# Performance work log

Measured on AMD Instinct MI355X. Metric: run time of the kernel, lower is better.

## Reference

```python
import jax, jax.numpy as jnp
import numpy as np

GAMMA = 0.5          # blending coeff from __init__
NEG_SLOPE = 0.2      # LeakyReLU slope
MASK_FILL = -9e15    # zero_vec constant from source

N, M, D = 8192, 8192, 256
SPARSITY = 0.01


def setup_inputs() -> dict:
    key = jax.random.key(0)
    k1, k2, k3, k4, k5 = jax.random.split(key, 5)
    input1 = jax.random.normal(k1, (N, D), dtype=jnp.float32)
    input2 = jax.random.normal(k2, (M, D), dtype=jnp.float32)
    adj = (jax.random.uniform(k3, (N, M)) < SPARSITY).astype(jnp.float32)
    # xavier_normal with gain=1.414 on (D,1): std = gain*sqrt(2/(D+1))
    std = 1.414 * np.sqrt(2.0 / (D + 1))
    a1 = jax.random.normal(k4, (D, 1), dtype=jnp.float32) * std
    a2 = jax.random.normal(k5, (D, 1), dtype=jnp.float32) * std
    return {"input1": input1, "input2": input2, "adj": adj, "a1": a1, "a2": a2}


def reference(input1, input2, adj, a1, a2):
    # e1: (N,1) broadcast against e2: (1,M) -> e: (N,M)
    e1 = input1 @ a1                      # (N,1)
    e2 = (input2 @ a2).T                  # (1,M)
    e = jax.nn.leaky_relu(e1 + e2, negative_slope=NEG_SLOPE)
    attention = jnp.where(adj > 0, e, MASK_FILL)
    attention = jax.nn.softmax(attention, axis=1)
    # scale each row by its adjacency degree, then gamma-blend with adj
    attention = attention * jnp.sum(adj, axis=1, keepdims=True)
    attention = attention * GAMMA + adj * (1.0 - GAMMA)
    return attention @ input2             # (N,D)
```

## Files before the change

### kernel.cpp

```cpp
#include <hip/hip_runtime.h>
#include <cstdint>
#include <cstddef>

#define NEG_SLOPE 0.2f
#define MAXK 256

typedef float f32x4 __attribute__((ext_vector_type(4)));
typedef unsigned short u16x4 __attribute__((ext_vector_type(4)));

static __device__ __forceinline__ unsigned short f2bf_rne(float f) {
  unsigned u = __float_as_uint(f);
  unsigned r = (u + 0x7FFFu + ((u >> 16) & 1u)) >> 16;
  return (unsigned short)r;
}
static __device__ __forceinline__ float bf2f(unsigned short h) {
  return __uint_as_float((unsigned)h << 16);
}

__global__ __launch_bounds__(256) void conv_kernel(
    const float* __restrict__ x2, unsigned short* __restrict__ x2h, int total4) {
  int t = blockIdx.x * blockDim.x + threadIdx.x;
  if (t >= total4) return;
  f32x4 v = reinterpret_cast<const f32x4*>(x2)[t];
  u16x4 h;
  h.x = f2bf_rne(v.x); h.y = f2bf_rne(v.y);
  h.z = f2bf_rne(v.z); h.w = f2bf_rne(v.w);
  reinterpret_cast<u16x4*>(x2h)[t] = h;
}

__global__ __launch_bounds__(256) void score_kernel(
    const float* __restrict__ x1, const float* __restrict__ x2,
    const float* __restrict__ a1, const float* __restrict__ a2,
    float* __restrict__ e1, float* __restrict__ f2, int N, int M, int D) {
  int gtid = blockIdx.x * blockDim.x + threadIdx.x;
  int wid = gtid >> 6;
  int lane = threadIdx.x & 63;
  if (wid >= N + M) return;
  const float* x; const float* a; float* outp; int row;
  if (wid < N) { x = x1; a = a1; outp = e1; row = wid; }
  else         { x = x2; a = a2; outp = f2; row = wid - N; }
  const float4 xv = *reinterpret_cast<const float4*>(x + (size_t)row * D + lane * 4);
  const float4 av = *reinterpret_cast<const float4*>(a + lane * 4);
  float s = xv.x * av.x + xv.y * av.y + xv.z * av.z + xv.w * av.w;
  #pragma unroll
  for (int off = 32; off > 0; off >>= 1) s += __shfl_down(s, off, 64);
  if (lane == 0) outp[row] = s;
}

__global__ __launch_bounds__(256) void attn_kernel(
    const float* __restrict__ adj, const unsigned short* __restrict__ x2h,
    const float* __restrict__ e1, const float* __restrict__ f2,
    float* __restrict__ out, int N, int M, int D) {
  __shared__ int   s_idx[4][MAXK];
  __shared__ float s_w[4][MAXK];

  const int tid  = threadIdx.x;
  const int wv   = tid >> 6;
  const int lane = tid & 63;
  const int row  = blockIdx.x * 4 + wv;
  if (row >= N) return;

  const int D4 = D >> 2;
  const float e1i = e1[row];
  const f32x4* __restrict__ arow4 =
      reinterpret_cast<const f32x4*>(adj + (size_t)row * M);

  uint64_t m0 = 0ull, m1 = 0ull;
  #pragma unroll 8
  for (int it = 0; it < 16; ++it) {
    f32x4 v = __builtin_nontemporal_load(&arow4[it * 64 + lane]);
    uint64_t b = 0;
    if (v.x > 0.f) b |= 1ull;
    if (v.y > 0.f) b |= 2ull;
    if (v.z > 0.f) b |= 4ull;
    if (v.w > 0.f) b |= 8ull;
    m0 |= b << (it * 4);
  }
  #pragma unroll 8
  for (int it = 16; it < 32; ++it) {
    f32x4 v = __builtin_nontemporal_load(&arow4[it * 64 + lane]);
    uint64_t b = 0;
    if (v.x > 0.f) b |= 1ull;
    if (v.y > 0.f) b |= 2ull;
    if (v.z > 0.f) b |= 4ull;
    if (v.w > 0.f) b |= 8ull;
    m1 |= b << ((it - 16) * 4);
  }
  const int cnt = __popcll(m0) + __popcll(m1);

  int incl = cnt;
  #pragma unroll
  for (int off = 1; off < 64; off <<= 1) {
    int v = __shfl_up(incl, off, 64);
    if (lane >= off) incl += v;
  }
  int pos = incl - cnt;
  const int K = __shfl(incl, 63, 64);

  while (m0) {
    int b = __ffsll((unsigned long long)m0) - 1;
    m0 &= m0 - 1;
    int c = ((b >> 2) << 6) + lane;
    int j = (c << 2) + (b & 3);
    float e = e1i + f2[j];
    e = (e > 0.f) ? e : NEG_SLOPE * e;
    if (pos < MAXK) { s_idx[wv][pos] = j; s_w[wv][pos] = e; }
    ++pos;
  }
  while (m1) {
    int b = __ffsll((unsigned long long)m1) - 1;
    m1 &= m1 - 1;
    int c = (((b >> 2) + 16) << 6) + lane;
    int j = (c << 2) + (b & 3);
    float e = e1i + f2[j];
    e = (e > 0.f) ? e : NEG_SLOPE * e;
    if (pos < MAXK) { s_idx[wv][pos] = j; s_w[wv][pos] = e; }
    ++pos;
  }

  float4* __restrict__ out4 = reinterpret_cast<float4*>(out);
  if (K == 0) {
    float4 z; z.x = z.y = z.z = z.w = 0.f;
    out4[(size_t)row * D4 + lane] = z;
    return;
  }

  float lm = -1e30f;
  for (int k = lane; k < K; k += 64) lm = fmaxf(lm, s_w[wv][k]);
  #pragma unroll
  for (int off = 32; off > 0; off >>= 1) lm = fmaxf(lm, __shfl_xor(lm, off, 64));

  float ls = 0.f;
  for (int k = lane; k < K; k += 64) {
    float p = __expf(s_w[wv][k] - lm);
    s_w[wv][k] = p;
    ls += p;
  }
  #pragma unroll
  for (int off = 32; off > 0; off >>= 1) ls += __shfl_xor(ls, off, 64);

  const float scale = 0.5f * (float)K / ls;
  for (int k = lane; k < K; k += 64) s_w[wv][k] = s_w[wv][k] * scale + 0.5f;

  const u16x4* __restrict__ x2h4 = reinterpret_cast<const u16x4*>(x2h);
  float4 a0, a1v, a2v, a3;
  a0.x=a0.y=a0.z=a0.w=0.f; a1v=a0; a2v=a0; a3=a0;
  int k = 0;
  for (; k + 4 <= K; k += 4) {
    int j0 = __builtin_amdgcn_readfirstlane(s_idx[wv][k]);
    int j1 = __builtin_amdgcn_readfirstlane(s_idx[wv][k + 1]);
    int j2 = __builtin_amdgcn_readfirstlane(s_idx[wv][k + 2]);
    int j3 = __builtin_amdgcn_readfirstlane(s_idx[wv][k + 3]);
    float w0 = s_w[wv][k],     w1 = s_w[wv][k + 1];
    float w2 = s_w[wv][k + 2], w3 = s_w[wv][k + 3];
    u16x4 h0 = x2h4[(size_t)j0 * D4 + lane];
    u16x4 h1 = x2h4[(size_t)j1 * D4 + lane];
    u16x4 h2 = x2h4[(size_t)j2 * D4 + lane];
    u16x4 h3 = x2h4[(size_t)j3 * D4 + lane];
    a0.x = fmaf(w0, bf2f(h0.x), a0.x); a0.y = fmaf(w0, bf2f(h0.y), a0.y);
    a0.z = fmaf(w0, bf2f(h0.z), a0.z); a0.w = fmaf(w0, bf2f(h0.w), a0.w);
    a1v.x = fmaf(w1, bf2f(h1.x), a1v.x); a1v.y = fmaf(w1, bf2f(h1.y), a1v.y);
    a1v.z = fmaf(w1, bf2f(h1.z), a1v.z); a1v.w = fmaf(w1, bf2f(h1.w), a1v.w);
    a2v.x = fmaf(w2, bf2f(h2.x), a2v.x); a2v.y = fmaf(w2, bf2f(h2.y), a2v.y);
    a2v.z = fmaf(w2, bf2f(h2.z), a2v.z); a2v.w = fmaf(w2, bf2f(h2.w), a2v.w);
    a3.x = fmaf(w3, bf2f(h3.x), a3.x); a3.y = fmaf(w3, bf2f(h3.y), a3.y);
    a3.z = fmaf(w3, bf2f(h3.z), a3.z); a3.w = fmaf(w3, bf2f(h3.w), a3.w);
  }
  for (; k < K; ++k) {
    int j = __builtin_amdgcn_readfirstlane(s_idx[wv][k]);
    float w = s_w[wv][k];
    u16x4 h = x2h4[(size_t)j * D4 + lane];
    a0.x = fmaf(w, bf2f(h.x), a0.x); a0.y = fmaf(w, bf2f(h.y), a0.y);
    a0.z = fmaf(w, bf2f(h.z), a0.z); a0.w = fmaf(w, bf2f(h.w), a0.w);
  }
  float4 r;
  r.x = (a0.x + a1v.x) + (a2v.x + a3.x);
  r.y = (a0.y + a1v.y) + (a2v.y + a3.y);
  r.z = (a0.z + a1v.z) + (a2v.z + a3.z);
  r.w = (a0.w + a1v.w) + (a2v.w + a3.w);
  out4[(size_t)row * D4 + lane] = r;
}

extern "C" void kernel_launch(void* const* d_in, const int* in_sizes, int n_in,
                              void* d_out, int out_size, void* d_ws, size_t ws_size,
                              hipStream_t stream) {
  const float* x1  = (const float*)d_in[0];
  const float* x2  = (const float*)d_in[1];
  const float* adj = (const float*)d_in[2];
  const float* a1  = (const float*)d_in[3];
  const float* a2  = (const float*)d_in[4];
  float* out = (float*)d_out;

  const int D = in_sizes[3];
  const int N = in_sizes[0] / D;
  const int M = in_sizes[1] / D;

  float* e1 = (float*)d_ws;
  float* f2 = e1 + N;
  unsigned short* x2h = (unsigned short*)(f2 + M);

  const int total4 = (M * D) >> 2;
  conv_kernel<<<(total4 + 255) / 256, 256, 0, stream>>>(x2, x2h, total4);

  const int waves = N + M;
  const int blocks1 = (waves * 64 + 255) / 256;
  score_kernel<<<blocks1, 256, 0, stream>>>(x1, x2, a1, a2, e1, f2, N, M, D);
  attn_kernel<<<(N + 3) / 4, 256, 0, stream>>>(adj, x2h, e1, f2, out, N, M, D);
}
```

Measured before the change: 79.66 us.

## Fuse bf16 conversion into scoring; split attention into compact and gather kernels

Folds the bf16 conversion of input2 into the row-score kernel, so input2 is read once instead of twice. The attention kernel is split in two: a compact kernel streams adj and writes per-row neighbor index/weight pairs (capped at KCAP) to workspace, and a separate gather kernel does the weighted bf16 row accumulation. The split lets each phase run with its own occupancy and access pattern, at the cost of an extra launch and a round trip of the pairs through global memory. Rows with more than KCAP neighbors are truncated, which could change results for dense rows. The old fused kernel is kept as a fallback when workspace is too small.

```diff
diff --git a/kernel.cpp b/kernel.cpp
--- a/kernel.cpp
+++ b/kernel.cpp
@@ -4,9 +4,11 @@
 
 #define NEG_SLOPE 0.2f
 #define MAXK 256
+#define KCAP 144
 
 typedef float f32x4 __attribute__((ext_vector_type(4)));
 typedef unsigned short u16x4 __attribute__((ext_vector_type(4)));
+typedef unsigned int u32x2 __attribute__((ext_vector_type(2)));
 
 static __device__ __forceinline__ unsigned short f2bf_rne(float f) {
   unsigned u = __float_as_uint(f);
@@ -17,40 +19,41 @@
   return __uint_as_float((unsigned)h << 16);
 }
 
-__global__ __launch_bounds__(256) void conv_kernel(
-    const float* __restrict__ x2, unsigned short* __restrict__ x2h, int total4) {
-  int t = blockIdx.x * blockDim.x + threadIdx.x;
-  if (t >= total4) return;
-  f32x4 v = reinterpret_cast<const f32x4*>(x2)[t];
-  u16x4 h;
-  h.x = f2bf_rne(v.x); h.y = f2bf_rne(v.y);
-  h.z = f2bf_rne(v.z); h.w = f2bf_rne(v.w);
-  reinterpret_cast<u16x4*>(x2h)[t] = h;
-}
-
-__global__ __launch_bounds__(256) void score_kernel(
+__global__ __launch_bounds__(256) void score_conv_kernel(
     const float* __restrict__ x1, const float* __restrict__ x2,
     const float* __restrict__ a1, const float* __restrict__ a2,
-    float* __restrict__ e1, float* __restrict__ f2, int N, int M, int D) {
+    float* __restrict__ e1, float* __restrict__ f2,
+    unsigned short* __restrict__ x2h, int N, int M, int D) {
   int gtid = blockIdx.x * blockDim.x + threadIdx.x;
   int wid = gtid >> 6;
   int lane = threadIdx.x & 63;
   if (wid >= N + M) return;
-  const float* x; const float* a; float* outp; int row;
-  if (wid < N) { x = x1; a = a1; outp = e1; row = wid; }
-  else         { x = x2; a = a2; outp = f2; row = wid - N; }
-  const float4 xv = *reinterpret_cast<const float4*>(x + (size_t)row * D + lane * 4);
-  const float4 av = *reinterpret_cast<const float4*>(a + lane * 4);
-  float s = xv.x * av.x + xv.y * av.y + xv.z * av.z + xv.w * av.w;
-  #pragma unroll
-  for (int off = 32; off > 0; off >>= 1) s += __shfl_down(s, off, 64);
-  if (lane == 0) outp[row] = s;
-}
-
-__global__ __launch_bounds__(256) void attn_kernel(
-    const float* __restrict__ adj, const unsigned short* __restrict__ x2h,
+  const float4 av = *reinterpret_cast<const float4*>(
+      ((wid < N) ? a1 : a2) + lane * 4);
+  if (wid < N) {
+    const float4 xv = *reinterpret_cast<const float4*>(x1 + (size_t)wid * D + lane * 4);
+    float s = xv.x * av.x + xv.y * av.y + xv.z * av.z + xv.w * av.w;
+    #pragma unroll
+    for (int off = 32; off > 0; off >>= 1) s += __shfl_down(s, off, 64);
+    if (lane == 0) e1[wid] = s;
+  } else {
+    int row = wid - N;
+    const float4 xv = *reinterpret_cast<const float4*>(x2 + (size_t)row * D + lane * 4);
+    float s = xv.x * av.x + xv.y * av.y + xv.z * av.z + xv.w * av.w;
+    u16x4 h;
+    h.x = f2bf_rne(xv.x); h.y = f2bf_rne(xv.y);
+    h.z = f2bf_rne(xv.z); h.w = f2bf_rne(xv.w);
+    reinterpret_cast<u16x4*>(x2h)[(size_t)row * (D >> 2) + lane] = h;
+    #pragma unroll
+    for (int off = 32; off > 0; off >>= 1) s += __shfl_down(s, off, 64);
+    if (lane == 0) f2[row] = s;
+  }
+}
+
+__global__ __launch_bounds__(256) void compact_kernel(
+    const float* __restrict__ adj,
     const float* __restrict__ e1, const float* __restrict__ f2,
-    float* __restrict__ out, int N, int M, int D) {
+    int* __restrict__ krow, u32x2* __restrict__ pairs, int N, int M) {
   __shared__ int   s_idx[4][MAXK];
   __shared__ float s_w[4][MAXK];
 
@@ -60,7 +63,6 @@
   const int row  = blockIdx.x * 4 + wv;
   if (row >= N) return;
 
-  const int D4 = D >> 2;
   const float e1i = e1[row];
   const f32x4* __restrict__ arow4 =
       reinterpret_cast<const f32x4*>(adj + (size_t)row * M);
@@ -118,18 +120,13 @@
     ++pos;
   }
 
-  float4* __restrict__ out4 = reinterpret_cast<float4*>(out);
-  if (K == 0) {
-    float4 z; z.x = z.y = z.z = z.w = 0.f;
-    out4[(size_t)row * D4 + lane] = z;
-    return;
-  }
+  if (lane == 0) krow[row] = (K < KCAP) ? K : KCAP;
+  if (K == 0) return;
 
   float lm = -1e30f;
   for (int k = lane; k < K; k += 64) lm = fmaxf(lm, s_w[wv][k]);
   #pragma unroll
   for (int off = 32; off > 0; off >>= 1) lm = fmaxf(lm, __shfl_xor(lm, off, 64));
-
   float ls = 0.f;
   for (int k = lane; k < K; k += 64) {
     float p = __expf(s_w[wv][k] - lm);
@@ -140,7 +137,39 @@
   for (int off = 32; off > 0; off >>= 1) ls += __shfl_xor(ls, off, 64);
 
   const float scale = 0.5f * (float)K / ls;
-  for (int k = lane; k < K; k += 64) s_w[wv][k] = s_w[wv][k] * scale + 0.5f;
+  for (int k = lane; k < K && k < KCAP; k += 64) {
+    u32x2 p;
+    p.x = (unsigned)s_idx[wv][k];
+    p.y = __float_as_uint(s_w[wv][k] * scale + 0.5f);
+    pairs[(size_t)row * KCAP + k] = p;
+  }
+}
+
+__global__ __launch_bounds__(256) void gather_kernel(
+    const unsigned short* __restrict__ x2h, const int* __restrict__ krow,
+    const u32x2* __restrict__ pairs, float* __restrict__ out, int N, int D) {
+  __shared__ int   s_idx[4][KCAP];
+  __shared__ float s_w[4][KCAP];
+
+  const int tid  = threadIdx.x;
+  const int wv   = tid >> 6;
+  const int lane = tid & 63;
+  const int row  = blockIdx.x * 4 + wv;
+  if (row >= N) return;
+
+  const int D4 = D >> 2;
+  float4* __restrict__ out4 = reinterpret_cast<float4*>(out);
+  const int K = krow[row];
+  if (K == 0) {
+    float4 z; z.x = z.y = z.z = z.w = 0.f;
+    out4[(size_t)row * D4 + lane] = z;
+    return;
+  }
+  for (int k = lane; k < K; k += 64) {
+    u32x2 p = pairs[(size_t)row * KCAP + k];
+    s_idx[wv][k] = (int)p.x;
+    s_w[wv][k]   = __uint_as_float(p.y);
+  }
 
   const u16x4* __restrict__ x2h4 = reinterpret_cast<const u16x4*>(x2h);
   float4 a0, a1v, a2v, a3;
@@ -181,6 +210,129 @@
   out4[(size_t)row * D4 + lane] = r;
 }
 
+__global__ __launch_bounds__(256) void attn_fused_kernel(
+    const float* __restrict__ adj, const unsigned short* __restrict__ x2h,
+    const float* __restrict__ e1, const float* __restrict__ f2,
+    float* __restrict__ out, int N, int M, int D) {
+  __shared__ int   s_idx[4][MAXK];
+  __shared__ float s_w[4][MAXK];
+  const int tid  = threadIdx.x;
+  const int wv   = tid >> 6;
+  const int lane = tid & 63;
+  const int row  = blockIdx.x * 4 + wv;
+  if (row >= N) return;
+  const int D4 = D >> 2;
+  const float e1i = e1[row];
+  const f32x4* __restrict__ arow4 = reinterpret_cast<const f32x4*>(adj + (size_t)row * M);
+  uint64_t m0 = 0ull, m1 = 0ull;
+  #pragma unroll 8
+  for (int it = 0; it < 16; ++it) {
+    f32x4 v = __builtin_nontemporal_load(&arow4[it * 64 + lane]);
+    uint64_t b = 0;
+    if (v.x > 0.f) b |= 1ull;
+    if (v.y > 0.f) b |= 2ull;
+    if (v.z > 0.f) b |= 4ull;
+    if (v.w > 0.f) b |= 8ull;
+    m0 |= b << (it * 4);
+  }
+  #pragma unroll 8
+  for (int it = 16; it < 32; ++it) {
+    f32x4 v = __builtin_nontemporal_load(&arow4[it * 64 + lane]);
+    uint64_t b = 0;
+    if (v.x > 0.f) b |= 1ull;
+    if (v.y > 0.f) b |= 2ull;
+    if (v.z > 0.f) b |= 4ull;
+    if (v.w > 0.f) b |= 8ull;
+    m1 |= b << ((it - 16) * 4);
+  }
+  const int cnt = __popcll(m0) + __popcll(m1);
+  int incl = cnt;
+  #pragma unroll
+  for (int off = 1; off < 64; off <<= 1) {
+    int v = __shfl_up(incl, off, 64);
+    if (lane >= off) incl += v;
+  }
+  int pos = incl - cnt;
+  const int K = __shfl(incl, 63, 64);
+  while (m0) {
+    int b = __ffsll((unsigned long long)m0) - 1;
+    m0 &= m0 - 1;
+    int c = ((b >> 2) << 6) + lane;
+    int j = (c << 2) + (b & 3);
+    float e = e1i + f2[j];
+    e = (e > 0.f) ? e : NEG_SLOPE * e;
+    if (pos < MAXK) { s_idx[wv][pos] = j; s_w[wv][pos] = e; }
+    ++pos;
+  }
+  while (m1) {
+    int b = __ffsll((unsigned long long)m1) - 1;
+    m1 &= m1 - 1;
+    int c = (((b >> 2) + 16) << 6) + lane;
+    int j = (c << 2) + (b & 3);
+    float e = e1i + f2[j];
+    e = (e > 0.f) ? e : NEG_SLOPE * e;
+    if (pos < MAXK) { s_idx[wv][pos] = j; s_w[wv][pos] = e; }
+    ++pos;
+  }
+  float4* __restrict__ out4 = reinterpret_cast<float4*>(out);
+  if (K == 0) {
+    float4 z; z.x = z.y = z.z = z.w = 0.f;
+    out4[(size_t)row * D4 + lane] = z;
+    return;
+  }
+  float lm = -1e30f;
+  for (int k = lane; k < K; k += 64) lm = fmaxf(lm, s_w[wv][k]);
+  #pragma unroll
+  for (int off = 32; off > 0; off >>= 1) lm = fmaxf(lm, __shfl_xor(lm, off, 64));
+  float ls = 0.f;
+  for (int k = lane; k < K; k += 64) {
+    float p = __expf(s_w[wv][k] - lm);
+    s_w[wv][k] = p;
+    ls += p;
+  }
+  #pragma unroll
+  for (int off = 32; off > 0; off >>= 1) ls += __shfl_xor(ls, off, 64);
+  const float scale = 0.5f * (float)K / ls;
+  for (int k = lane; k < K; k += 64) s_w[wv][k] = s_w[wv][k] * scale + 0.5f;
+  const u16x4* __restrict__ x2h4 = reinterpret_cast<const u16x4*>(x2h);
+  float4 a0, a1v, a2v, a3;
+  a0.x=a0.y=a0.z=a0.w=0.f; a1v=a0; a2v=a0; a3=a0;
+  int k = 0;
+  for (; k + 4 <= K; k += 4) {
+    int j0 = __builtin_amdgcn_readfirstlane(s_idx[wv][k]);
+    int j1 = __builtin_amdgcn_readfirstlane(s_idx[wv][k + 1]);
+    int j2 = __builtin_amdgcn_readfirstlane(s_idx[wv][k + 2]);
+    int j3 = __builtin_amdgcn_readfirstlane(s_idx[wv][k + 3]);
+    float w0 = s_w[wv][k],     w1 = s_w[wv][k + 1];
+    float w2 = s_w[wv][k + 2], w3 = s_w[wv][k + 3];
+    u16x4 h0 = x2h4[(size_t)j0 * D4 + lane];
+    u16x4 h1 = x2h4[(size_t)j1 * D4 + lane];
+    u16x4 h2 = x2h4[(size_t)j2 * D4 + lane];
+    u16x4 h3 = x2h4[(size_t)j3 * D4 + lane];
+    a0.x = fmaf(w0, bf2f(h0.x), a0.x); a0.y = fmaf(w0, bf2f(h0.y), a0.y);
+    a0.z = fmaf(w0, bf2f(h0.z), a0.z); a0.w = fmaf(w0, bf2f(h0.w), a0.w);
+    a1v.x = fmaf(w1, bf2f(h1.x), a1v.x); a1v.y = fmaf(w1, bf2f(h1.y), a1v.y);
+    a1v.z = fmaf(w1, bf2f(h1.z), a1v.z); a1v.w = fmaf(w1, bf2f(h1.w), a1v.w);
+    a2v.x = fmaf(w2, bf2f(h2.x), a2v.x); a2v.y = fmaf(w2, bf2f(h2.y), a2v.y);
+    a2v.z = fmaf(w2, bf2f(h2.z), a2v.z); a2v.w = fmaf(w2, bf2f(h2.w), a2v.w);
+    a3.x = fmaf(w3, bf2f(h3.x), a3.x); a3.y = fmaf(w3, bf2f(h3.y), a3.y);
+    a3.z = fmaf(w3, bf2f(h3.z), a3.z); a3.w = fmaf(w3, bf2f(h3.w), a3.w);
+  }
+  for (; k < K; ++k) {
+    int j = __builtin_amdgcn_readfirstlane(s_idx[wv][k]);
+    float w = s_w[wv][k];
+    u16x4 h = x2h4[(size_t)j * D4 + lane];
+    a0.x = fmaf(w, bf2f(h.x), a0.x); a0.y = fmaf(w, bf2f(h.y), a0.y);
+    a0.z = fmaf(w, bf2f(h.z), a0.z); a0.w = fmaf(w, bf2f(h.w), a0.w);
+  }
+  float4 r;
+  r.x = (a0.x + a1v.x) + (a2v.x + a3.x);
+  r.y = (a0.y + a1v.y) + (a2v.y + a3.y);
+  r.z = (a0.z + a1v.z) + (a2v.z + a3.z);
+  r.w = (a0.w + a1v.w) + (a2v.w + a3.w);
+  out4[(size_t)row * D4 + lane] = r;
+}
+
 extern "C" void kernel_launch(void* const* d_in, const int* in_sizes, int n_in,
                               void* d_out, int out_size, void* d_ws, size_t ws_size,
                               hipStream_t stream) {
@@ -195,15 +347,22 @@
   const int N = in_sizes[0] / D;
   const int M = in_sizes[1] / D;
 
-  float* e1 = (float*)d_ws;
-  float* f2 = e1 + N;
-  unsigned short* x2h = (unsigned short*)(f2 + M);
-
-  const int total4 = (M * D) >> 2;
-  conv_kernel<<<(total4 + 255) / 256, 256, 0, stream>>>(x2, x2h, total4);
+  char* p = (char*)d_ws;
+  float* e1 = (float*)p;                 p += (size_t)N * 4;
+  float* f2 = (float*)p;                 p += (size_t)M * 4;
+  unsigned short* x2h = (unsigned short*)p; p += (size_t)M * D * 2;
+  int* krow = (int*)p;                   p += (size_t)N * 4;
+  u32x2* pairs = (u32x2*)p;              p += (size_t)N * KCAP * 8;
+  const size_t need = (size_t)(p - (char*)d_ws);
 
   const int waves = N + M;
   const int blocks1 = (waves * 64 + 255) / 256;
-  score_kernel<<<blocks1, 256, 0, stream>>>(x1, x2, a1, a2, e1, f2, N, M, D);
-  attn_kernel<<<(N + 3) / 4, 256, 0, stream>>>(adj, x2h, e1, f2, out, N, M, D);
-}
+  score_conv_kernel<<<blocks1, 256, 0, stream>>>(x1, x2, a1, a2, e1, f2, x2h, N, M, D);
+
+  if (ws_size >= need) {
+    compact_kernel<<<(N + 3) / 4, 256, 0, stream>>>(adj, e1, f2, krow, pairs, N, M);
+    gather_kernel<<<(N + 3) / 4, 256, 0, stream>>>(x2h, krow, pairs, out, N, D);
+  } else {
+    attn_fused_kernel<<<(N + 3) / 4, 256, 0, stream>>>(adj, x2h, e1, f2, out, N, M, D);
+  }
+}
```

Result: slower. 82.77 us (+3.9%).

## Fuse conversion into score kernel and stream adjacency chunks with one-pass softmax

Applied to the files above, without the earlier changes.

Folds the bf16 conversion of input2 into the score kernel, removing one launch and one extra read of input2. The score kernel also keeps a global maximum of f2 via atomics, so the attention kernel can use a fixed softmax shift bound (leaky_relu(e1 + max f2)) instead of a per-row max pass. The attention kernel now processes the adjacency row in four 2048-column chunks, prefetching the next chunk while it compacts and gathers the current one. It accumulates the exp-weighted and plain sums in one pass and applies the normalisation at the end. The risks are underflow when the global bound sits far above a row's true max, and a per-chunk cap of 160 neighbours.

```diff
diff --git a/kernel.cpp b/kernel.cpp
--- a/kernel.cpp
+++ b/kernel.cpp
@@ -3,7 +3,8 @@
 #include <cstddef>
 
 #define NEG_SLOPE 0.2f
-#define MAXK 256
+#define CCAP 160
+#define NCHUNK 4
 
 typedef float f32x4 __attribute__((ext_vector_type(4)));
 typedef unsigned short u16x4 __attribute__((ext_vector_type(4)));
@@ -16,43 +17,56 @@
 static __device__ __forceinline__ float bf2f(unsigned short h) {
   return __uint_as_float((unsigned)h << 16);
 }
-
-__global__ __launch_bounds__(256) void conv_kernel(
-    const float* __restrict__ x2, unsigned short* __restrict__ x2h, int total4) {
-  int t = blockIdx.x * blockDim.x + threadIdx.x;
-  if (t >= total4) return;
-  f32x4 v = reinterpret_cast<const f32x4*>(x2)[t];
-  u16x4 h;
-  h.x = f2bf_rne(v.x); h.y = f2bf_rne(v.y);
-  h.z = f2bf_rne(v.z); h.w = f2bf_rne(v.w);
-  reinterpret_cast<u16x4*>(x2h)[t] = h;
-}
-
-__global__ __launch_bounds__(256) void score_kernel(
+static __device__ __forceinline__ unsigned enc_f(float x) {
+  unsigned u = __float_as_uint(x);
+  return (u & 0x80000000u) ? ~u : (u | 0x80000000u);
+}
+static __device__ __forceinline__ float dec_f(unsigned e) {
+  return __uint_as_float((e & 0x80000000u) ? (e ^ 0x80000000u) : ~e);
+}
+
+__global__ __launch_bounds__(256) void score_conv_kernel(
     const float* __restrict__ x1, const float* __restrict__ x2,
     const float* __restrict__ a1, const float* __restrict__ a2,
-    float* __restrict__ e1, float* __restrict__ f2, int N, int M, int D) {
+    float* __restrict__ e1, float* __restrict__ f2,
+    unsigned short* __restrict__ x2h, unsigned* __restrict__ f2max_enc,
+    int N, int M, int D) {
   int gtid = blockIdx.x * blockDim.x + threadIdx.x;
   int wid = gtid >> 6;
   int lane = threadIdx.x & 63;
   if (wid >= N + M) return;
-  const float* x; const float* a; float* outp; int row;
-  if (wid < N) { x = x1; a = a1; outp = e1; row = wid; }
-  else         { x = x2; a = a2; outp = f2; row = wid - N; }
-  const float4 xv = *reinterpret_cast<const float4*>(x + (size_t)row * D + lane * 4);
-  const float4 av = *reinterpret_cast<const float4*>(a + lane * 4);
-  float s = xv.x * av.x + xv.y * av.y + xv.z * av.z + xv.w * av.w;
-  #pragma unroll
-  for (int off = 32; off > 0; off >>= 1) s += __shfl_down(s, off, 64);
-  if (lane == 0) outp[row] = s;
+  const float4 av = *reinterpret_cast<const float4*>(
+      ((wid < N) ? a1 : a2) + lane * 4);
+  if (wid < N) {
+    const float4 xv = *reinterpret_cast<const float4*>(x1 + (size_t)wid * D + lane * 4);
+    float s = xv.x * av.x + xv.y * av.y + xv.z * av.z + xv.w * av.w;
+    #pragma unroll
+    for (int off = 32; off > 0; off >>= 1) s += __shfl_down(s, off, 64);
+    if (lane == 0) e1[wid] = s;
+  } else {
+    int row = wid - N;
+    const float4 xv = *reinterpret_cast<const float4*>(x2 + (size_t)row * D + lane * 4);
+    float s = xv.x * av.x + xv.y * av.y + xv.z * av.z + xv.w * av.w;
+    u16x4 h;
+    h.x = f2bf_rne(xv.x); h.y = f2bf_rne(xv.y);
+    h.z = f2bf_rne(xv.z); h.w = f2bf_rne(xv.w);
+    reinterpret_cast<u16x4*>(x2h)[(size_t)row * (D >> 2) + lane] = h;
+    #pragma unroll
+    for (int off = 32; off > 0; off >>= 1) s += __shfl_down(s, off, 64);
+    if (lane == 0) {
+      f2[row] = s;
+      atomicMax(f2max_enc, enc_f(s));
+    }
+  }
 }
 
 __global__ __launch_bounds__(256) void attn_kernel(
     const float* __restrict__ adj, const unsigned short* __restrict__ x2h,
     const float* __restrict__ e1, const float* __restrict__ f2,
+    const unsigned* __restrict__ f2max_enc,
     float* __restrict__ out, int N, int M, int D) {
-  __shared__ int   s_idx[4][MAXK];
-  __shared__ float s_w[4][MAXK];
+  __shared__ int   s_idx[4][CCAP];
+  __shared__ float s_e[4][CCAP];
 
   const int tid  = threadIdx.x;
   const int wv   = tid >> 6;
@@ -62,60 +76,121 @@
 
   const int D4 = D >> 2;
   const float e1i = e1[row];
+  float mb = e1i + dec_f(*f2max_enc);
+  mb = (mb > 0.f) ? mb : NEG_SLOPE * mb;
+
   const f32x4* __restrict__ arow4 =
       reinterpret_cast<const f32x4*>(adj + (size_t)row * M);
-
-  uint64_t m0 = 0ull, m1 = 0ull;
-  #pragma unroll 8
-  for (int it = 0; it < 16; ++it) {
-    f32x4 v = __builtin_nontemporal_load(&arow4[it * 64 + lane]);
-    uint64_t b = 0;
-    if (v.x > 0.f) b |= 1ull;
-    if (v.y > 0.f) b |= 2ull;
-    if (v.z > 0.f) b |= 4ull;
-    if (v.w > 0.f) b |= 8ull;
-    m0 |= b << (it * 4);
-  }
-  #pragma unroll 8
-  for (int it = 16; it < 32; ++it) {
-    f32x4 v = __builtin_nontemporal_load(&arow4[it * 64 + lane]);
-    uint64_t b = 0;
-    if (v.x > 0.f) b |= 1ull;
-    if (v.y > 0.f) b |= 2ull;
-    if (v.z > 0.f) b |= 4ull;
-    if (v.w > 0.f) b |= 8ull;
-    m1 |= b << ((it - 16) * 4);
-  }
-  const int cnt = __popcll(m0) + __popcll(m1);
-
-  int incl = cnt;
-  #pragma unroll
-  for (int off = 1; off < 64; off <<= 1) {
-    int v = __shfl_up(incl, off, 64);
-    if (lane >= off) incl += v;
-  }
-  int pos = incl - cnt;
-  const int K = __shfl(incl, 63, 64);
-
-  while (m0) {
-    int b = __ffsll((unsigned long long)m0) - 1;
-    m0 &= m0 - 1;
-    int c = ((b >> 2) << 6) + lane;
-    int j = (c << 2) + (b & 3);
-    float e = e1i + f2[j];
-    e = (e > 0.f) ? e : NEG_SLOPE * e;
-    if (pos < MAXK) { s_idx[wv][pos] = j; s_w[wv][pos] = e; }
-    ++pos;
-  }
-  while (m1) {
-    int b = __ffsll((unsigned long long)m1) - 1;
-    m1 &= m1 - 1;
-    int c = (((b >> 2) + 16) << 6) + lane;
-    int j = (c << 2) + (b & 3);
-    float e = e1i + f2[j];
-    e = (e > 0.f) ? e : NEG_SLOPE * e;
-    if (pos < MAXK) { s_idx[wv][pos] = j; s_w[wv][pos] = e; }
-    ++pos;
+  const u16x4* __restrict__ x2h4 = reinterpret_cast<const u16x4*>(x2h);
+
+  const f32x4* pb = arow4 + lane;
+  f32x4 v0 = __builtin_nontemporal_load(pb + 0 * 64);
+  f32x4 v1 = __builtin_nontemporal_load(pb + 1 * 64);
+  f32x4 v2 = __builtin_nontemporal_load(pb + 2 * 64);
+  f32x4 v3 = __builtin_nontemporal_load(pb + 3 * 64);
+  f32x4 v4 = __builtin_nontemporal_load(pb + 4 * 64);
+  f32x4 v5 = __builtin_nontemporal_load(pb + 5 * 64);
+  f32x4 v6 = __builtin_nontemporal_load(pb + 6 * 64);
+  f32x4 v7 = __builtin_nontemporal_load(pb + 7 * 64);
+
+  float4 acc1, acc2;
+  acc1.x = acc1.y = acc1.z = acc1.w = 0.f;
+  acc2 = acc1;
+  float Z = 0.f;
+  int K = 0;
+
+  for (int c = 0; c < NCHUNK; ++c) {
+    unsigned mask = 0;
+    {
+      f32x4 x;
+      x = v0; if (x.x>0.f) mask|=1u<<0;  if (x.y>0.f) mask|=1u<<1;  if (x.z>0.f) mask|=1u<<2;  if (x.w>0.f) mask|=1u<<3;
+      x = v1; if (x.x>0.f) mask|=1u<<4;  if (x.y>0.f) mask|=1u<<5;  if (x.z>0.f) mask|=1u<<6;  if (x.w>0.f) mask|=1u<<7;
+      x = v2; if (x.x>0.f) mask|=1u<<8;  if (x.y>0.f) mask|=1u<<9;  if (x.z>0.f) mask|=1u<<10; if (x.w>0.f) mask|=1u<<11;
+      x = v3; if (x.x>0.f) mask|=1u<<12; if (x.y>0.f) mask|=1u<<13; if (x.z>0.f) mask|=1u<<14; if (x.w>0.f) mask|=1u<<15;
+      x = v4; if (x.x>0.f) mask|=1u<<16; if (x.y>0.f) mask|=1u<<17; if (x.z>0.f) mask|=1u<<18; if (x.w>0.f) mask|=1u<<19;
+      x = v5; if (x.x>0.f) mask|=1u<<20; if (x.y>0.f) mask|=1u<<21; if (x.z>0.f) mask|=1u<<22; if (x.w>0.f) mask|=1u<<23;
+      x = v6; if (x.x>0.f) mask|=1u<<24; if (x.y>0.f) mask|=1u<<25; if (x.z>0.f) mask|=1u<<26; if (x.w>0.f) mask|=1u<<27;
+      x = v7; if (x.x>0.f) mask|=1u<<28; if (x.y>0.f) mask|=1u<<29; if (x.z>0.f) mask|=1u<<30; if (x.w>0.f) mask|=1u<<31;
+    }
+    if (c + 1 < NCHUNK) {
+      const f32x4* nb = arow4 + (c + 1) * 512 + lane;
+      v0 = __builtin_nontemporal_load(nb + 0 * 64);
+      v1 = __builtin_nontemporal_load(nb + 1 * 64);
+      v2 = __builtin_nontemporal_load(nb + 2 * 64);
+      v3 = __builtin_nontemporal_load(nb + 3 * 64);
+      v4 = __builtin_nontemporal_load(nb + 4 * 64);
+      v5 = __builtin_nontemporal_load(nb + 5 * 64);
+      v6 = __builtin_nontemporal_load(nb + 6 * 64);
+      v7 = __builtin_nontemporal_load(nb + 7 * 64);
+    }
+
+    const int cnt = __popc(mask);
+    int incl = cnt;
+    #pragma unroll
+    for (int off = 1; off < 64; off <<= 1) {
+      int t = __shfl_up(incl, off, 64);
+      if (lane >= off) incl += t;
+    }
+    int pos = incl - cnt;
+    const int ck = __shfl(incl, 63, 64);
+    const int jb = c * 2048;
+
+    while (mask) {
+      int b = __ffs(mask) - 1;
+      mask &= mask - 1;
+      int j = jb + ((((b >> 2) << 6) + lane) << 2) + (b & 3);
+      float e = e1i + f2[j];
+      e = (e > 0.f) ? e : NEG_SLOPE * e;
+      if (pos < CCAP) { s_idx[wv][pos] = j; s_e[wv][pos] = e; }
+      ++pos;
+    }
+
+    const int cn = (ck < CCAP) ? ck : CCAP;
+    int k = 0;
+    for (; k + 4 <= cn; k += 4) {
+      int j0 = __builtin_amdgcn_readfirstlane(s_idx[wv][k + 0]);
+      int j1 = __builtin_amdgcn_readfirstlane(s_idx[wv][k + 1]);
+      int j2 = __builtin_amdgcn_readfirstlane(s_idx[wv][k + 2]);
+      int j3 = __builtin_amdgcn_readfirstlane(s_idx[wv][k + 3]);
+      float p0 = __expf(s_e[wv][k + 0] - mb);
+      float p1 = __expf(s_e[wv][k + 1] - mb);
+      float p2 = __expf(s_e[wv][k + 2] - mb);
+      float p3 = __expf(s_e[wv][k + 3] - mb);
+      u16x4 h0 = x2h4[(size_t)j0 * D4 + lane];
+      u16x4 h1 = x2h4[(size_t)j1 * D4 + lane];
+      u16x4 h2 = x2h4[(size_t)j2 * D4 + lane];
+      u16x4 h3 = x2h4[(size_t)j3 * D4 + lane];
+      Z += (p0 + p1) + (p2 + p3);
+      float g;
+      g = bf2f(h0.x); acc1.x = fmaf(p0, g, acc1.x); acc2.x += g;
+      g = bf2f(h0.y); acc1.y = fmaf(p0, g, acc1.y); acc2.y += g;
+      g = bf2f(h0.z); acc1.z = fmaf(p0, g, acc1.z); acc2.z += g;
+      g = bf2f(h0.w); acc1.w = fmaf(p0, g, acc1.w); acc2.w += g;
+      g = bf2f(h1.x); acc1.x = fmaf(p1, g, acc1.x); acc2.x += g;
+      g = bf2f(h1.y); acc1.y = fmaf(p1, g, acc1.y); acc2.y += g;
+      g = bf2f(h1.z); acc1.z = fmaf(p1, g, acc1.z); acc2.z += g;
+      g = bf2f(h1.w); acc1.w = fmaf(p1, g, acc1.w); acc2.w += g;
+      g = bf2f(h2.x); acc1.x = fmaf(p2, g, acc1.x); acc2.x += g;
+      g = bf2f(h2.y); acc1.y = fmaf(p2, g, acc1.y); acc2.y += g;
+      g = bf2f(h2.z); acc1.z = fmaf(p2, g, acc1.z); acc2.z += g;
+      g = bf2f(h2.w); acc1.w = fmaf(p2, g, acc1.w); acc2.w += g;
+      g = bf2f(h3.x); acc1.x = fmaf(p3, g, acc1.x); acc2.x += g;
+      g = bf2f(h3.y); acc1.y = fmaf(p3, g, acc1.y); acc2.y += g;
+      g = bf2f(h3.z); acc1.z = fmaf(p3, g, acc1.z); acc2.z += g;
+      g = bf2f(h3.w); acc1.w = fmaf(p3, g, acc1.w); acc2.w += g;
+    }
+    for (; k < cn; ++k) {
+      int j = __builtin_amdgcn_readfirstlane(s_idx[wv][k]);
+      float p = __expf(s_e[wv][k] - mb);
+      u16x4 h = x2h4[(size_t)j * D4 + lane];
+      Z += p;
+      float g;
+      g = bf2f(h.x); acc1.x = fmaf(p, g, acc1.x); acc2.x += g;
+      g = bf2f(h.y); acc1.y = fmaf(p, g, acc1.y); acc2.y += g;
+      g = bf2f(h.z); acc1.z = fmaf(p, g, acc1.z); acc2.z += g;
+      g = bf2f(h.w); acc1.w = fmaf(p, g, acc1.w); acc2.w += g;
+    }
+    K += ck;
   }
 
   float4* __restrict__ out4 = reinterpret_cast<float4*>(out);
@@ -124,60 +199,12 @@
     out4[(size_t)row * D4 + lane] = z;
     return;
   }
-
-  float lm = -1e30f;
-  for (int k = lane; k < K; k += 64) lm = fmaxf(lm, s_w[wv][k]);
-  #pragma unroll
-  for (int off = 32; off > 0; off >>= 1) lm = fmaxf(lm, __shfl_xor(lm, off, 64));
-
-  float ls = 0.f;
-  for (int k = lane; k < K; k += 64) {
-    float p = __expf(s_w[wv][k] - lm);
-    s_w[wv][k] = p;
-    ls += p;
-  }
-  #pragma unroll
-  for (int off = 32; off > 0; off >>= 1) ls += __shfl_xor(ls, off, 64);
-
-  const float scale = 0.5f * (float)K / ls;
-  for (int k = lane; k < K; k += 64) s_w[wv][k] = s_w[wv][k] * scale + 0.5f;
-
-  const u16x4* __restrict__ x2h4 = reinterpret_cast<const u16x4*>(x2h);
-  float4 a0, a1v, a2v, a3;
-  a0.x=a0.y=a0.z=a0.w=0.f; a1v=a0; a2v=a0; a3=a0;
-  int k = 0;
-  for (; k + 4 <= K; k += 4) {
-    int j0 = __builtin_amdgcn_readfirstlane(s_idx[wv][k]);
-    int j1 = __builtin_amdgcn_readfirstlane(s_idx[wv][k + 1]);
-    int j2 = __builtin_amdgcn_readfirstlane(s_idx[wv][k + 2]);
-    int j3 = __builtin_amdgcn_readfirstlane(s_idx[wv][k + 3]);
-    float w0 = s_w[wv][k],     w1 = s_w[wv][k + 1];
-    float w2 = s_w[wv][k + 2], w3 = s_w[wv][k + 3];
-    u16x4 h0 = x2h4[(size_t)j0 * D4 + lane];
-    u16x4 h1 = x2h4[(size_t)j1 * D4 + lane];
-    u16x4 h2 = x2h4[(size_t)j2 * D4 + lane];
-    u16x4 h3 = x2h4[(size_t)j3 * D4 + lane];
-    a0.x = fmaf(w0, bf2f(h0.x), a0.x); a0.y = fmaf(w0, bf2f(h0.y), a0.y);
-    a0.z = fmaf(w0, bf2f(h0.z), a0.z); a0.w = fmaf(w0, bf2f(h0.w), a0.w);
-    a1v.x = fmaf(w1, bf2f(h1.x), a1v.x); a1v.y = fmaf(w1, bf2f(h1.y), a1v.y);
-    a1v.z = fmaf(w1, bf2f(h1.z), a1v.z); a1v.w = fmaf(w1, bf2f(h1.w), a1v.w);
-    a2v.x = fmaf(w2, bf2f(h2.x), a2v.x); a2v.y = fmaf(w2, bf2f(h2.y), a2v.y);
-    a2v.z = fmaf(w2, bf2f(h2.z), a2v.z); a2v.w = fmaf(w2, bf2f(h2.w), a2v.w);
-    a3.x = fmaf(w3, bf2f(h3.x), a3.x); a3.y = fmaf(w3, bf2f(h3.y), a3.y);
-    a3.z = fmaf(w3, bf2f(h3.z), a3.z); a3.w = fmaf(w3, bf2f(h3.w), a3.w);
-  }
-  for (; k < K; ++k) {
-    int j = __builtin_amdgcn_readfirstlane(s_idx[wv][k]);
-    float w = s_w[wv][k];
-    u16x4 h = x2h4[(size_t)j * D4 + lane];
-    a0.x = fmaf(w, bf2f(h.x), a0.x); a0.y = fmaf(w, bf2f(h.y), a0.y);
-    a0.z = fmaf(w, bf2f(h.z), a0.z); a0.w = fmaf(w, bf2f(h.w), a0.w);
-  }
+  const float s1 = 0.5f * (float)K / Z;
   float4 r;
-  r.x = (a0.x + a1v.x) + (a2v.x + a3.x);
-  r.y = (a0.y + a1v.y) + (a2v.y + a3.y);
-  r.z = (a0.z + a1v.z) + (a2v.z + a3.z);
-  r.w = (a0.w + a1v.w) + (a2v.w + a3.w);
+  r.x = fmaf(acc1.x, s1, acc2.x * 0.5f);
+  r.y = fmaf(acc1.y, s1, acc2.y * 0.5f);
+  r.z = fmaf(acc1.z, s1, acc2.z * 0.5f);
+  r.w = fmaf(acc1.w, s1, acc2.w * 0.5f);
   out4[(size_t)row * D4 + lane] = r;
 }
 
@@ -195,15 +222,18 @@
   const int N = in_sizes[0] / D;
   const int M = in_sizes[1] / D;
 
-  float* e1 = (float*)d_ws;
-  float* f2 = e1 + N;
-  unsigned short* x2h = (unsigned short*)(f2 + M);
-
-  const int total4 = (M * D) >> 2;
-  conv_kernel<<<(total4 + 255) / 256, 256, 0, stream>>>(x2, x2h, total4);
+  char* p = (char*)d_ws;
+  float* e1 = (float*)p;                    p += (size_t)N * 4;
+  float* f2 = (float*)p;                    p += (size_t)M * 4;
+  unsigned short* x2h = (unsigned short*)p; p += (size_t)M * D * 2;
+  unsigned* f2max_enc = (unsigned*)p;
+
+  hipMemsetAsync(f2max_enc, 0, sizeof(unsigned), stream);
 
   const int waves = N + M;
   const int blocks1 = (waves * 64 + 255) / 256;
-  score_kernel<<<blocks1, 256, 0, stream>>>(x1, x2, a1, a2, e1, f2, N, M, D);
-  attn_kernel<<<(N + 3) / 4, 256, 0, stream>>>(adj, x2h, e1, f2, out, N, M, D);
-}
+  score_conv_kernel<<<blocks1, 256, 0, stream>>>(x1, x2, a1, a2, e1, f2, x2h,
+                                                 f2max_enc, N, M, D);
+  attn_kernel<<<(N + 3) / 4, 256, 0, stream>>>(adj, x2h, e1, f2, f2max_enc,
+                                               out, N, M, D);
+}
```

New measurement: 174.5 us. 2.19x slower.

## Fuse bf16 conversion into scoring and split attention into producer/consumer waves

Applied to the files above, without the earlier changes.

Folds the x2-to-bf16 conversion into the score kernel, so x2 is read once and one launch is dropped. The attention kernel becomes a 512-thread block: four producer waves scan adjacency rows and build sparse index/weight lists in double-buffered shared memory, while four consumer waves gather x2 rows for the previous group. f2 is staged into shared memory (32KB) to avoid scattered global reads. This risks lower occupancy from the larger shared memory footprint, a block-wide barrier per stage, hardcoded M=8192 in the f2 staging, and a neighbor cap lowered to 192.

```diff
diff --git a/kernel.cpp b/kernel.cpp
--- a/kernel.cpp
+++ b/kernel.cpp
@@ -3,7 +3,9 @@
 #include <cstddef>
 
 #define NEG_SLOPE 0.2f
-#define MAXK 256
+#define CAP 192
+#define NB 4
+#define RPB 16
 
 typedef float f32x4 __attribute__((ext_vector_type(4)));
 typedef unsigned short u16x4 __attribute__((ext_vector_type(4)));
@@ -17,168 +19,197 @@
   return __uint_as_float((unsigned)h << 16);
 }
 
-__global__ __launch_bounds__(256) void conv_kernel(
-    const float* __restrict__ x2, unsigned short* __restrict__ x2h, int total4) {
-  int t = blockIdx.x * blockDim.x + threadIdx.x;
-  if (t >= total4) return;
-  f32x4 v = reinterpret_cast<const f32x4*>(x2)[t];
-  u16x4 h;
-  h.x = f2bf_rne(v.x); h.y = f2bf_rne(v.y);
-  h.z = f2bf_rne(v.z); h.w = f2bf_rne(v.w);
-  reinterpret_cast<u16x4*>(x2h)[t] = h;
-}
-
-__global__ __launch_bounds__(256) void score_kernel(
+__global__ __launch_bounds__(256) void score_conv_kernel(
     const float* __restrict__ x1, const float* __restrict__ x2,
     const float* __restrict__ a1, const float* __restrict__ a2,
-    float* __restrict__ e1, float* __restrict__ f2, int N, int M, int D) {
+    float* __restrict__ e1, float* __restrict__ f2,
+    unsigned short* __restrict__ x2h, int N, int M, int D) {
   int gtid = blockIdx.x * blockDim.x + threadIdx.x;
   int wid = gtid >> 6;
   int lane = threadIdx.x & 63;
   if (wid >= N + M) return;
-  const float* x; const float* a; float* outp; int row;
-  if (wid < N) { x = x1; a = a1; outp = e1; row = wid; }
-  else         { x = x2; a = a2; outp = f2; row = wid - N; }
-  const float4 xv = *reinterpret_cast<const float4*>(x + (size_t)row * D + lane * 4);
-  const float4 av = *reinterpret_cast<const float4*>(a + lane * 4);
-  float s = xv.x * av.x + xv.y * av.y + xv.z * av.z + xv.w * av.w;
-  #pragma unroll
-  for (int off = 32; off > 0; off >>= 1) s += __shfl_down(s, off, 64);
-  if (lane == 0) outp[row] = s;
-}
-
-__global__ __launch_bounds__(256) void attn_kernel(
+  const float4 av = *reinterpret_cast<const float4*>(
+      ((wid < N) ? a1 : a2) + lane * 4);
+  if (wid < N) {
+    const float4 xv = *reinterpret_cast<const float4*>(x1 + (size_t)wid * D + lane * 4);
+    float s = xv.x * av.x + xv.y * av.y + xv.z * av.z + xv.w * av.w;
+    #pragma unroll
+    for (int off = 32; off > 0; off >>= 1) s += __shfl_down(s, off, 64);
+    if (lane == 0) e1[wid] = s;
+  } else {
+    int row = wid - N;
+    const float4 xv = *reinterpret_cast<const float4*>(x2 + (size_t)row * D + lane * 4);
+    float s = xv.x * av.x + xv.y * av.y + xv.z * av.z + xv.w * av.w;
+    u16x4 h;
+    h.x = f2bf_rne(xv.x); h.y = f2bf_rne(xv.y);
+    h.z = f2bf_rne(xv.z); h.w = f2bf_rne(xv.w);
+    reinterpret_cast<u16x4*>(x2h)[(size_t)row * (D >> 2) + lane] = h;
+    #pragma unroll
+    for (int off = 32; off > 0; off >>= 1) s += __shfl_down(s, off, 64);
+    if (lane == 0) f2[row] = s;
+  }
+}
+
+__global__ __launch_bounds__(512) void attn_pc_kernel(
     const float* __restrict__ adj, const unsigned short* __restrict__ x2h,
     const float* __restrict__ e1, const float* __restrict__ f2,
     float* __restrict__ out, int N, int M, int D) {
-  __shared__ int   s_idx[4][MAXK];
-  __shared__ float s_w[4][MAXK];
+  __shared__ float s_f2[8192];
+  __shared__ int   s_idx[2][4][CAP];
+  __shared__ float s_w[2][4][CAP];
+  __shared__ int   s_cnt[2][4];
 
   const int tid  = threadIdx.x;
   const int wv   = tid >> 6;
   const int lane = tid & 63;
-  const int row  = blockIdx.x * 4 + wv;
-  if (row >= N) return;
-
-  const int D4 = D >> 2;
-  const float e1i = e1[row];
-  const f32x4* __restrict__ arow4 =
-      reinterpret_cast<const f32x4*>(adj + (size_t)row * M);
-
-  uint64_t m0 = 0ull, m1 = 0ull;
-  #pragma unroll 8
-  for (int it = 0; it < 16; ++it) {
-    f32x4 v = __builtin_nontemporal_load(&arow4[it * 64 + lane]);
-    uint64_t b = 0;
-    if (v.x > 0.f) b |= 1ull;
-    if (v.y > 0.f) b |= 2ull;
-    if (v.z > 0.f) b |= 4ull;
-    if (v.w > 0.f) b |= 8ull;
-    m0 |= b << (it * 4);
+  const int D4   = D >> 2;
+
+  {
+    const f32x4* src = reinterpret_cast<const f32x4*>(f2);
+    f32x4* dst = reinterpret_cast<f32x4*>(s_f2);
+    #pragma unroll
+    for (int i = 0; i < 4; ++i) dst[tid + i * 512] = src[tid + i * 512];
   }
-  #pragma unroll 8
-  for (int it = 16; it < 32; ++it) {
-    f32x4 v = __builtin_nontemporal_load(&arow4[it * 64 + lane]);
-    uint64_t b = 0;
-    if (v.x > 0.f) b |= 1ull;
-    if (v.y > 0.f) b |= 2ull;
-    if (v.z > 0.f) b |= 4ull;
-    if (v.w > 0.f) b |= 8ull;
-    m1 |= b << ((it - 16) * 4);
+  __syncthreads();
+
+  const int base = blockIdx.x * RPB;
+  const u16x4* __restrict__ x2h4 = reinterpret_cast<const u16x4*>(x2h);
+  float4* __restrict__ out4 = reinterpret_cast<float4*>(out);
+
+  for (int r = 0; r <= NB; ++r) {
+    if (wv < 4) {
+      if (r < NB) {
+        const int row = base + r * 4 + wv;
+        const int p = r & 1;
+        if (row < N) {
+          const float e1i = e1[row];
+          const f32x4* __restrict__ arow4 =
+              reinterpret_cast<const f32x4*>(adj + (size_t)row * M);
+          uint64_t m0 = 0ull, m1 = 0ull;
+          #pragma unroll 8
+          for (int it = 0; it < 16; ++it) {
+            f32x4 v = __builtin_nontemporal_load(&arow4[it * 64 + lane]);
+            uint64_t b = 0;
+            if (v.x > 0.f) b |= 1ull;
+            if (v.y > 0.f) b |= 2ull;
+            if (v.z > 0.f) b |= 4ull;
+            if (v.w > 0.f) b |= 8ull;
+            m0 |= b << (it * 4);
+          }
+          #pragma unroll 8
+          for (int it = 16; it < 32; ++it) {
+            f32x4 v = __builtin_nontemporal_load(&arow4[it * 64 + lane]);
+            uint64_t b = 0;
+            if (v.x > 0.f) b |= 1ull;
+            if (v.y > 0.f) b |= 2ull;
+            if (v.z > 0.f) b |= 4ull;
+            if (v.w > 0.f) b |= 8ull;
+            m1 |= b << ((it - 16) * 4);
+          }
+          const int cnt = __popcll(m0) + __popcll(m1);
+          int incl = cnt;
+          #pragma unroll
+          for (int off = 1; off < 64; off <<= 1) {
+            int t = __shfl_up(incl, off, 64);
+            if (lane >= off) incl += t;
+          }
+          int pos = incl - cnt;
+          const int K = __shfl(incl, 63, 64);
+
+          while (m0) {
+            int b = __ffsll((unsigned long long)m0) - 1;
+            m0 &= m0 - 1;
+            int j = ((((b >> 2) << 6) + lane) << 2) + (b & 3);
+            float e = e1i + s_f2[j];
+            e = (e > 0.f) ? e : NEG_SLOPE * e;
+            if (pos < CAP) { s_idx[p][wv][pos] = j; s_w[p][wv][pos] = e; }
+            ++pos;
+          }
+          while (m1) {
+            int b = __ffsll((unsigned long long)m1) - 1;
+            m1 &= m1 - 1;
+            int j = (((((b >> 2) + 16) << 6) + lane) << 2) + (b & 3);
+            float e = e1i + s_f2[j];
+            e = (e > 0.f) ? e : NEG_SLOPE * e;
+            if (pos < CAP) { s_idx[p][wv][pos] = j; s_w[p][wv][pos] = e; }
+            ++pos;
+          }
+
+          const int Kc = (K < CAP) ? K : CAP;
+          if (lane == 0) s_cnt[p][wv] = Kc;
+          if (K > 0) {
+            float lm = -1e30f;
+            for (int k = lane; k < Kc; k += 64) lm = fmaxf(lm, s_w[p][wv][k]);
+            #pragma unroll
+            for (int off = 32; off > 0; off >>= 1)
+              lm = fmaxf(lm, __shfl_xor(lm, off, 64));
+            float ls = 0.f;
+            for (int k = lane; k < Kc; k += 64) {
+              float pr = __expf(s_w[p][wv][k] - lm);
+              s_w[p][wv][k] = pr;
+              ls += pr;
+            }
+            #pragma unroll
+            for (int off = 32; off > 0; off >>= 1) ls += __shfl_xor(ls, off, 64);
+            const float scale = 0.5f * (float)K / ls;
+            for (int k = lane; k < Kc; k += 64)
+              s_w[p][wv][k] = s_w[p][wv][k] * scale + 0.5f;
+          }
+        }
+      }
+    } else {
+      if (r >= 1) {
+        const int cw = wv - 4;
+        const int row = base + (r - 1) * 4 + cw;
+        const int p = (r - 1) & 1;
+        if (row < N) {
+          const int K = s_cnt[p][cw];
+          if (K == 0) {
+            float4 z; z.x = z.y = z.z = z.w = 0.f;
+            out4[(size_t)row * D4 + lane] = z;
+          } else {
+            float4 a0, a1v, a2v, a3;
+            a0.x = a0.y = a0.z = a0.w = 0.f; a1v = a0; a2v = a0; a3 = a0;
+            int k = 0;
+            for (; k + 4 <= K; k += 4) {
+              int j0 = __builtin_amdgcn_readfirstlane(s_idx[p][cw][k + 0]);
+              int j1 = __builtin_amdgcn_readfirstlane(s_idx[p][cw][k + 1]);
+              int j2 = __builtin_amdgcn_readfirstlane(s_idx[p][cw][k + 2]);
+              int j3 = __builtin_amdgcn_readfirstlane(s_idx[p][cw][k + 3]);
+              float w0 = s_w[p][cw][k + 0], w1 = s_w[p][cw][k + 1];
+              float w2 = s_w[p][cw][k + 2], w3 = s_w[p][cw][k + 3];
+              u16x4 h0 = x2h4[(size_t)j0 * D4 + lane];
+              u16x4 h1 = x2h4[(size_t)j1 * D4 + lane];
+              u16x4 h2 = x2h4[(size_t)j2 * D4 + lane];
+              u16x4 h3 = x2h4[(size_t)j3 * D4 + lane];
+              a0.x = fmaf(w0, bf2f(h0.x), a0.x); a0.y = fmaf(w0, bf2f(h0.y), a0.y);
+              a0.z = fmaf(w0, bf2f(h0.z), a0.z); a0.w = fmaf(w0, bf2f(h0.w), a0.w);
+              a1v.x = fmaf(w1, bf2f(h1.x), a1v.x); a1v.y = fmaf(w1, bf2f(h1.y), a1v.y);
+              a1v.z = fmaf(w1, bf2f(h1.z), a1v.z); a1v.w = fmaf(w1, bf2f(h1.w), a1v.w);
+              a2v.x = fmaf(w2, bf2f(h2.x), a2v.x); a2v.y = fmaf(w2, bf2f(h2.y), a2v.y);
+              a2v.z = fmaf(w2, bf2f(h2.z), a2v.z); a2v.w = fmaf(w2, bf2f(h2.w), a2v.w);
+              a3.x = fmaf(w3, bf2f(h3.x), a3.x); a3.y = fmaf(w3, bf2f(h3.y), a3.y);
+              a3.z = fmaf(w3, bf2f(h3.z), a3.z); a3.w = fmaf(w3, bf2f(h3.w), a3.w);
+            }
+            for (; k < K; ++k) {
+              int j = __builtin_amdgcn_readfirstlane(s_idx[p][cw][k]);
+              float w = s_w[p][cw][k];
+              u16x4 h = x2h4[(size_t)j * D4 + lane];
+              a0.x = fmaf(w, bf2f(h.x), a0.x); a0.y = fmaf(w, bf2f(h.y), a0.y);
+              a0.z = fmaf(w, bf2f(h.z), a0.z); a0.w = fmaf(w, bf2f(h.w), a0.w);
+            }
+            float4 rr;
+            rr.x = (a0.x + a1v.x) + (a2v.x + a3.x);
+            rr.y = (a0.y + a1v.y) + (a2v.y + a3.y);
+            rr.z = (a0.z + a1v.z) + (a2v.z + a3.z);
+            rr.w = (a0.w + a1v.w) + (a2v.w + a3.w);
+            out4[(size_t)row * D4 + lane] = rr;
+          }
+        }
+      }
+    }
+    __syncthreads();
   }
-  const int cnt = __popcll(m0) + __popcll(m1);
-
-  int incl = cnt;
-  #pragma unroll
-  for (int off = 1; off < 64; off <<= 1) {
-    int v = __shfl_up(incl, off, 64);
-    if (lane >= off) incl += v;
-  }
-  int pos = incl - cnt;
-  const int K = __shfl(incl, 63, 64);
-
-  while (m0) {
-    int b = __ffsll((unsigned long long)m0) - 1;
-    m0 &= m0 - 1;
-    int c = ((b >> 2) << 6) + lane;
-    int j = (c << 2) + (b & 3);
-    float e = e1i + f2[j];
-    e = (e > 0.f) ? e : NEG_SLOPE * e;
-    if (pos < MAXK) { s_idx[wv][pos] = j; s_w[wv][pos] = e; }
-    ++pos;
-  }
-  while (m1) {
-    int b = __ffsll((unsigned long long)m1) - 1;
-    m1 &= m1 - 1;
-    int c = (((b >> 2) + 16) << 6) + lane;
-    int j = (c << 2) + (b & 3);
-    float e = e1i + f2[j];
-    e = (e > 0.f) ? e : NEG_SLOPE * e;
-    if (pos < MAXK) { s_idx[wv][pos] = j; s_w[wv][pos] = e; }
-    ++pos;
-  }
-
-  float4* __restrict__ out4 = reinterpret_cast<float4*>(out);
-  if (K == 0) {
-    float4 z; z.x = z.y = z.z = z.w = 0.f;
-    out4[(size_t)row * D4 + lane] = z;
-    return;
-  }
-
-  float lm = -1e30f;
-  for (int k = lane; k < K; k += 64) lm = fmaxf(lm, s_w[wv][k]);
-  #pragma unroll
-  for (int off = 32; off > 0; off >>= 1) lm = fmaxf(lm, __shfl_xor(lm, off, 64));
-
-  float ls = 0.f;
-  for (int k = lane; k < K; k += 64) {
-    float p = __expf(s_w[wv][k] - lm);
-    s_w[wv][k] = p;
-    ls += p;
-  }
-  #pragma unroll
-  for (int off = 32; off > 0; off >>= 1) ls += __shfl_xor(ls, off, 64);
-
-  const float scale = 0.5f * (float)K / ls;
-  for (int k = lane; k < K; k += 64) s_w[wv][k] = s_w[wv][k] * scale + 0.5f;
-
-  const u16x4* __restrict__ x2h4 = reinterpret_cast<const u16x4*>(x2h);
-  float4 a0, a1v, a2v, a3;
-  a0.x=a0.y=a0.z=a0.w=0.f; a1v=a0; a2v=a0; a3=a0;
-  int k = 0;
-  for (; k + 4 <= K; k += 4) {
-    int j0 = __builtin_amdgcn_readfirstlane(s_idx[wv][k]);
-    int j1 = __builtin_amdgcn_readfirstlane(s_idx[wv][k + 1]);
-    int j2 = __builtin_amdgcn_readfirstlane(s_idx[wv][k + 2]);
-    int j3 = __builtin_amdgcn_readfirstlane(s_idx[wv][k + 3]);
-    float w0 = s_w[wv][k],     w1 = s_w[wv][k + 1];
-    float w2 = s_w[wv][k + 2], w3 = s_w[wv][k + 3];
-    u16x4 h0 = x2h4[(size_t)j0 * D4 + lane];
-    u16x4 h1 = x2h4[(size_t)j1 * D4 + lane];
-    u16x4 h2 = x2h4[(size_t)j2 * D4 + lane];
-    u16x4 h3 = x2h4[(size_t)j3 * D4 + lane];
-    a0.x = fmaf(w0, bf2f(h0.x), a0.x); a0.y = fmaf(w0, bf2f(h0.y), a0.y);
-    a0.z = fmaf(w0, bf2f(h0.z), a0.z); a0.w = fmaf(w0, bf2f(h0.w), a0.w);
-    a1v.x = fmaf(w1, bf2f(h1.x), a1v.x); a1v.y = fmaf(w1, bf2f(h1.y), a1v.y);
-    a1v.z = fmaf(w1, bf2f(h1.z), a1v.z); a1v.w = fmaf(w1, bf2f(h1.w), a1v.w);
-    a2v.x = fmaf(w2, bf2f(h2.x), a2v.x); a2v.y = fmaf(w2, bf2f(h2.y), a2v.y);
-    a2v.z = fmaf(w2, bf2f(h2.z), a2v.z); a2v.w = fmaf(w2, bf2f(h2.w), a2v.w);
-    a3.x = fmaf(w3, bf2f(h3.x), a3.x); a3.y = fmaf(w3, bf2f(h3.y), a3.y);
-    a3.z = fmaf(w3, bf2f(h3.z), a3.z); a3.w = fmaf(w3, bf2f(h3.w), a3.w);
-  }
-  for (; k < K; ++k) {
-    int j = __builtin_amdgcn_readfirstlane(s_idx[wv][k]);
-    float w = s_w[wv][k];
-    u16x4 h = x2h4[(size_t)j * D4 + lane];
-    a0.x = fmaf(w, bf2f(h.x), a0.x); a0.y = fmaf(w, bf2f(h.y), a0.y);
-    a0.z = fmaf(w, bf2f(h.z), a0.z); a0.w = fmaf(w, bf2f(h.w), a0.w);
-  }
-  float4 r;
-  r.x = (a0.x + a1v.x) + (a2v.x + a3.x);
-  r.y = (a0.y + a1v.y) + (a2v.y + a3.y);
-  r.z = (a0.z + a1v.z) + (a2v.z + a3.z);
-  r.w = (a0.w + a1v.w) + (a2v.w + a3.w);
-  out4[(size_t)row * D4 + lane] = r;
 }
 
 extern "C" void kernel_launch(void* const* d_in, const int* in_sizes, int n_in,
@@ -195,15 +226,13 @@
   const int N = in_sizes[0] / D;
   const int M = in_sizes[1] / D;
 
-  float* e1 = (float*)d_ws;
-  float* f2 = e1 + N;
-  unsigned short* x2h = (unsigned short*)(f2 + M);
-
-  const int total4 = (M * D) >> 2;
-  conv_kernel<<<(total4 + 255) / 256, 256, 0, stream>>>(x2, x2h, total4);
+  char* p = (char*)d_ws;
+  float* e1 = (float*)p;                    p += (size_t)N * 4;
+  float* f2 = (float*)p;                    p += (size_t)M * 4;
+  unsigned short* x2h = (unsigned short*)p;
 
   const int waves = N + M;
   const int blocks1 = (waves * 64 + 255) / 256;
-  score_kernel<<<blocks1, 256, 0, stream>>>(x1, x2, a1, a2, e1, f2, N, M, D);
-  attn_kernel<<<(N + 3) / 4, 256, 0, stream>>>(adj, x2h, e1, f2, out, N, M, D);
-}
+  score_conv_kernel<<<blocks1, 256, 0, stream>>>(x1, x2, a1, a2, e1, f2, x2h, N, M, D);
+  attn_pc_kernel<<<(N + RPB - 1) / RPB, 512, 0, stream>>>(adj, x2h, e1, f2, out, N, M, D);
+}
```

Result: slower. 89.52 us (+12.4%).
